# Performance work log

Hardware: AMD Instinct MI355X
Metric: run time of the kernel (lower is better)

## Reference

```python
import jax, jax.numpy as jnp
import numpy as np

H, W, WS, HEADS = 112, 112, 7, 8
DIM, HID = 512, 2048


def _layernorm(x, g, b, eps=1e-5):
    mu = jnp.mean(x, axis=-1, keepdims=True)
    var = jnp.var(x, axis=-1, keepdims=True)
    return (x - mu) * jax.lax.rsqrt(var + eps) * g + b


def _cpe(x, w, b):
    # depthwise 3x3 conv positional encoding with residual; x: [B, L, C]
    B, L, C = x.shape
    img = x.reshape(B, H, W, C)
    feat = jax.lax.conv_general_dilated(
        img, w, window_strides=(1, 1), padding='SAME',
        dimension_numbers=('NHWC', 'HWIO', 'NHWC'), feature_group_count=C) + b
    return x + feat.reshape(B, L, C)


def _window_partition(x):
    # [B, H, W, C] -> [B*nW, ws*ws, C]
    B, _, _, C = x.shape
    x = x.reshape(B, H // WS, WS, W // WS, WS, C)
    x = jnp.transpose(x, (0, 1, 3, 2, 4, 5))
    return x.reshape(-1, WS * WS, C)


def _window_reverse(xw, B):
    # [B*nW, ws*ws, C] -> [B, H*W, C]
    C = xw.shape[-1]
    x = xw.reshape(B, H // WS, W // WS, WS, WS, C)
    x = jnp.transpose(x, (0, 1, 3, 2, 4, 5))
    return x.reshape(B, H * W, C)


def _attention(x, qkv_w, qkv_b, proj_w, proj_b):
    # x: [nW, N, C]; standard MHA within each window
    nW, N, C = x.shape
    d = C // HEADS
    qkv = x @ qkv_w + qkv_b                      # [nW, N, 3C]
    qkv = qkv.reshape(nW, N, 3, HEADS, d)
    q, k, v = qkv[:, :, 0], qkv[:, :, 1], qkv[:, :, 2]  # [nW, N, h, d]
    scale = d ** -0.5
    attn = jnp.einsum('wqhd,wkhd->whqk', q * scale, k)
    attn = jax.nn.softmax(attn, axis=-1)
    out = jnp.einsum('whqk,wkhd->wqhd', attn, v).reshape(nW, N, C)
    return out @ proj_w + proj_b


def setup_inputs() -> dict:
    key = jax.random.key(0)
    ks = jax.random.split(key, 16)
    s = 0.02
    return {
        'x': jax.random.normal(ks[0], (4, H * W, DIM), jnp.float32),
        'cpe0_w': jax.random.normal(ks[1], (3, 3, 1, DIM), jnp.float32) * s,
        'cpe0_b': jnp.zeros((DIM,), jnp.float32),
        'cpe1_w': jax.random.normal(ks[2], (3, 3, 1, DIM), jnp.float32) * s,
        'cpe1_b': jnp.zeros((DIM,), jnp.float32),
        'ln1_g': jnp.ones((DIM,), jnp.float32),
        'ln1_b': jnp.zeros((DIM,), jnp.float32),
        'ln2_g': jnp.ones((DIM,), jnp.float32),
        'ln2_b': jnp.zeros((DIM,), jnp.float32),
        'qkv_w': jax.random.normal(ks[3], (DIM, 3 * DIM), jnp.float32) * s,
        'qkv_b': jnp.zeros((3 * DIM,), jnp.float32),
        'attn_proj_w': jax.random.normal(ks[4], (DIM, DIM), jnp.float32) * s,
        'attn_proj_b': jnp.zeros((DIM,), jnp.float32),
        'fc1_w': jax.random.normal(ks[5], (DIM, HID), jnp.float32) * s,
        'fc1_b': jnp.zeros((HID,), jnp.float32),
        'fc2_w': jax.random.normal(ks[6], (HID, DIM), jnp.float32) * s,
        'fc2_b': jnp.zeros((DIM,), jnp.float32),
    }


def reference(x, cpe0_w, cpe0_b, cpe1_w, cpe1_b, ln1_g, ln1_b, ln2_g, ln2_b,
              qkv_w, qkv_b, attn_proj_w, attn_proj_b, fc1_w, fc1_b, fc2_w, fc2_b):
    B, L, C = x.shape
    shortcut = _cpe(x, cpe0_w, cpe0_b)                 # CPE #1 (with residual)
    h = _layernorm(shortcut, ln1_g, ln1_b)
    h = _window_partition(h.reshape(B, H, W, C))       # [B*nW, 49, C]
    h = _attention(h, qkv_w, qkv_b, attn_proj_w, attn_proj_b)
    h = _window_reverse(h, B)                          # [B, L, C]
    h = shortcut + h
    h = _cpe(h, cpe1_w, cpe1_b)                        # CPE #2 (with residual)
    m = _layernorm(h, ln2_g, ln2_b)
    m = jax.nn.gelu(m @ fc1_w + fc1_b) @ fc2_w + fc2_b
    return h + m
```

## Files before the change

### kernel.cpp

```cpp
#include <hip/hip_runtime.h>
#include <stdint.h>

#define HH 112
#define WW 112
#define CC 512
#define BB 4
#define LLEN (HH*WW)
#define NTOK (BB*LLEN)
#define NHEADS 8
#define HD 64
#define HIDDEN 2048

typedef __bf16 bf16x8 __attribute__((ext_vector_type(8)));
typedef float f32x4 __attribute__((ext_vector_type(4)));
typedef int i32x8 __attribute__((ext_vector_type(8)));
typedef long i64;

__device__ __forceinline__ unsigned short f2bf(float x) {
  uint32_t u = __float_as_uint(x);
  u += 0x7fffu + ((u >> 16) & 1u);
  return (unsigned short)(u >> 16);
}
__device__ __forceinline__ float bf2f(unsigned short h) {
  return __uint_as_float((uint32_t)h << 16);
}
__device__ __forceinline__ int cvt4_fp8(float a, float b, float c, float d) {
  int r = 0;
  r = __builtin_amdgcn_cvt_pk_fp8_f32(a, b, r, false);
  r = __builtin_amdgcn_cvt_pk_fp8_f32(c, d, r, true);
  return r;
}

__device__ __forceinline__ void gload16(const void* gptr, void* lptr) {
  __builtin_amdgcn_global_load_lds(
      (const __attribute__((address_space(1))) void*)gptr,
      (__attribute__((address_space(3))) void*)lptr,
      16, 0, 0);
}

#define WAITV3() asm volatile("s_waitcnt vmcnt(3)" ::: "memory")
#define WAITV4() asm volatile("s_waitcnt vmcnt(4)" ::: "memory")
#define WAITV0() asm volatile("s_waitcnt vmcnt(0)" ::: "memory")
#define BAR() __builtin_amdgcn_s_barrier()
#define WAITL() do { asm volatile("s_waitcnt lgkmcnt(0)" ::: "memory"); \
                     __builtin_amdgcn_sched_barrier(0); } while (0)

__global__ __launch_bounds__(256) void wtall_kernel(
    const float* __restrict__ qkv_w, const float* __restrict__ proj_w,
    const float* __restrict__ fc1_w, const float* __restrict__ fc2_w,
    unsigned char* __restrict__ o0, unsigned char* __restrict__ o1,
    unsigned char* __restrict__ o2, unsigned char* __restrict__ o3) {
  int idx = blockIdx.x * 256 + threadIdx.x;
  const float* w; unsigned char* o; int K, N;
  if (idx < 786432)        { w = qkv_w;  o = o0; K = 512;  N = 1536; }
  else if (idx < 1048576)  { w = proj_w; o = o1; K = 512;  N = 512;  idx -= 786432; }
  else if (idx < 2097152)  { w = fc1_w;  o = o2; K = 512;  N = 2048; idx -= 1048576; }
  else                     { w = fc2_w;  o = o3; K = 2048; N = 512;  idx -= 2097152; }
  int n = idx / K, k = idx - n * K;
  float v = w[(size_t)k * N + n] * 32.f;
  int r = __builtin_amdgcn_cvt_pk_fp8_f32(v, v, 0, false);
  o[idx] = (unsigned char)r;
}

template <int INBF>
__global__ __launch_bounds__(256) void cpe_ln_kernel(
    const void* __restrict__ xin, const float* __restrict__ w,
    const float* __restrict__ bias, const float* __restrict__ lng,
    const float* __restrict__ lnb, unsigned short* __restrict__ outB,
    unsigned char* __restrict__ ln8) {
  const int wid = threadIdx.x >> 6;
  const int lane = threadIdx.x & 63;
  const int xx = blockIdx.x * 4 + wid;
  const int yy = blockIdx.y;
  const int bb = blockIdx.z;
  const int c = lane * 8;

  float acc[8];
  {
    float4 b0 = *(const float4*)(&bias[c]);
    float4 b1 = *(const float4*)(&bias[c + 4]);
    acc[0] = b0.x; acc[1] = b0.y; acc[2] = b0.z; acc[3] = b0.w;
    acc[4] = b1.x; acc[5] = b1.y; acc[6] = b1.z; acc[7] = b1.w;
  }
  float xv[8];

  #pragma unroll
  for (int ky = 0; ky < 3; ky++) {
    int y = yy + ky - 1;
    bool yok = (unsigned)y < (unsigned)HH;
    #pragma unroll
    for (int kx = 0; kx < 3; kx++) {
      int x2 = xx + kx - 1;
      bool ok = yok && ((unsigned)x2 < (unsigned)WW);
      float v[8];
      if (ok) {
        size_t eo = (((size_t)bb * HH + y) * WW + x2) * CC + c;
        if (INBF) {
          uint4 u = *(const uint4*)(&((const unsigned short*)xin)[eo]);
          v[0] = bf2f((unsigned short)(u.x & 0xffff)); v[1] = bf2f((unsigned short)(u.x >> 16));
          v[2] = bf2f((unsigned short)(u.y & 0xffff)); v[3] = bf2f((unsigned short)(u.y >> 16));
          v[4] = bf2f((unsigned short)(u.z & 0xffff)); v[5] = bf2f((unsigned short)(u.z >> 16));
          v[6] = bf2f((unsigned short)(u.w & 0xffff)); v[7] = bf2f((unsigned short)(u.w >> 16));
        } else {
          float4 a = *(const float4*)(&((const float*)xin)[eo]);
          float4 b = *(const float4*)(&((const float*)xin)[eo + 4]);
          v[0] = a.x; v[1] = a.y; v[2] = a.z; v[3] = a.w;
          v[4] = b.x; v[5] = b.y; v[6] = b.z; v[7] = b.w;
        }
      } else {
        #pragma unroll
        for (int e = 0; e < 8; e++) v[e] = 0.f;
      }
      if (ky == 1 && kx == 1) {
        #pragma unroll
        for (int e = 0; e < 8; e++) xv[e] = v[e];
      }
      float4 w0 = *(const float4*)(&w[(ky * 3 + kx) * CC + c]);
      float4 w1 = *(const float4*)(&w[(ky * 3 + kx) * CC + c + 4]);
      acc[0] = fmaf(v[0], w0.x, acc[0]); acc[1] = fmaf(v[1], w0.y, acc[1]);
      acc[2] = fmaf(v[2], w0.z, acc[2]); acc[3] = fmaf(v[3], w0.w, acc[3]);
      acc[4] = fmaf(v[4], w1.x, acc[4]); acc[5] = fmaf(v[5], w1.y, acc[5]);
      acc[6] = fmaf(v[6], w1.z, acc[6]); acc[7] = fmaf(v[7], w1.w, acc[7]);
    }
  }

  float r[8];
  #pragma unroll
  for (int e = 0; e < 8; e++) r[e] = xv[e] + acc[e];

  const size_t o = (((size_t)bb * HH + yy) * WW + xx) * CC + c;
  {
    uint4 pk;
    pk.x = (uint32_t)f2bf(r[0]) | ((uint32_t)f2bf(r[1]) << 16);
    pk.y = (uint32_t)f2bf(r[2]) | ((uint32_t)f2bf(r[3]) << 16);
    pk.z = (uint32_t)f2bf(r[4]) | ((uint32_t)f2bf(r[5]) << 16);
    pk.w = (uint32_t)f2bf(r[6]) | ((uint32_t)f2bf(r[7]) << 16);
    *(uint4*)(&outB[o]) = pk;
  }

  float s = 0.f, ss = 0.f;
  #pragma unroll
  for (int e = 0; e < 8; e++) { s += r[e]; ss += r[e] * r[e]; }
  #pragma unroll
  for (int of = 32; of; of >>= 1) {
    s += __shfl_xor(s, of, 64);
    ss += __shfl_xor(ss, of, 64);
  }
  float mu = s * (1.f / CC);
  float var = ss * (1.f / CC) - mu * mu;
  float rsd = rsqrtf(var + 1e-5f);
  float4 g0 = *(const float4*)(&lng[c]);
  float4 g1 = *(const float4*)(&lng[c + 4]);
  float4 b0 = *(const float4*)(&lnb[c]);
  float4 b1 = *(const float4*)(&lnb[c + 4]);
  float gv[8] = {g0.x, g0.y, g0.z, g0.w, g1.x, g1.y, g1.z, g1.w};
  float bv[8] = {b0.x, b0.y, b0.z, b0.w, b1.x, b1.y, b1.z, b1.w};
  float ov[8];
  #pragma unroll
  for (int e = 0; e < 8; e++) ov[e] = (r[e] - mu) * rsd * gv[e] + bv[e];
  uint2 pk8;
  pk8.x = (uint32_t)cvt4_fp8(ov[0], ov[1], ov[2], ov[3]);
  pk8.y = (uint32_t)cvt4_fp8(ov[4], ov[5], ov[6], ov[7]);
  *(uint2*)(&ln8[o]) = pk8;
}

#define BM 256
#define BN 128
#define BK8 64

template <int MODE, int K>
__global__ __launch_bounds__(512) void gemm8_kernel(
    const unsigned char* __restrict__ A, const unsigned char* __restrict__ BT,
    const float* __restrict__ bias, const unsigned short* __restrict__ resB,
    unsigned short* __restrict__ outB16, int M, int N) {
  __shared__ unsigned char ldsb[49152];
  int nwg = gridDim.x * gridDim.y;
  int flat = blockIdx.y * gridDim.x + blockIdx.x;
  int swz = (flat & 7) * (nwg >> 3) + (flat >> 3);
  int bx = swz % gridDim.x, by = swz / gridDim.x;
  const int bm = by * BM, bn = bx * BN;
  const int t = threadIdx.x;
  const int wid = t >> 6, lane = t & 63;
  const int wr = wid >> 1, wc = wid & 1;
  const int lr = lane & 15, g = lane >> 4;
  const int swr = (lr >> 1) & 3;
  const int rb0 = (((g >> 1)      ) ^ swr) * 16 + (g & 1) * 8;
  const int rb1 = (((g >> 1) + 2) ^ swr) * 16 + (g & 1) * 8;
  const int srow = t >> 2;
  const int scol = (((t & 3) ^ ((t >> 3) & 3)) & 3) * 16;
  const size_t arow0 = (size_t)(bm + srow) * K + scol;
  const size_t arow1 = (size_t)(bm + 128 + srow) * K + scol;
  const size_t brow  = (size_t)(bn + srow) * K + scol;
  const int ldso = wid * 1024;

#define STG8(b, kt) do { \
    gload16(&A[arow0 + (kt)], ldsb + (b) * 16384 + ldso); \
    gload16(&A[arow1 + (kt)], ldsb + (b) * 16384 + 8192 + ldso); \
    gload16(&BT[brow + (kt)], ldsb + 32768 + (b) * 8192 + ldso); } while (0)

  f32x4 acc[4][4] = {};
  constexpr int nt = K / BK8;

  STG8(0, 0);
  STG8(1, BK8);

  #pragma unroll
  for (int tile = 0; tile < nt - 1; ++tile) {
    WAITV3(); BAR();
    const unsigned char* as = ldsb + (tile & 1) * 16384;
    const unsigned char* bs = ldsb + 32768 + (tile & 1) * 8192;
    i64 af0[4], af1[4], bf0[4], bf1[4];
    #pragma unroll
    for (int i = 0; i < 4; i++) {
      const unsigned char* p = &as[(wr * 64 + i * 16 + lr) * BK8];
      af0[i] = *(const i64*)(p + rb0);
      af1[i] = *(const i64*)(p + rb1);
    }
    #pragma unroll
    for (int j = 0; j < 4; j++) {
      const unsigned char* p = &bs[(wc * 64 + j * 16 + lr) * BK8];
      bf0[j] = *(const i64*)(p + rb0);
      bf1[j] = *(const i64*)(p + rb1);
    }
    WAITL();
    BAR();
    if (tile + 2 < nt) STG8(tile & 1, (tile + 2) * BK8);
    __builtin_amdgcn_s_setprio(1);
    #pragma unroll
    for (int i = 0; i < 4; i++)
      #pragma unroll
      for (int j = 0; j < 4; j++) {
        acc[i][j] = __builtin_amdgcn_mfma_f32_16x16x32_fp8_fp8(af0[i], bf0[j], acc[i][j], 0, 0, 0);
        acc[i][j] = __builtin_amdgcn_mfma_f32_16x16x32_fp8_fp8(af1[i], bf1[j], acc[i][j], 0, 0, 0);
      }
    __builtin_amdgcn_s_setprio(0);
  }
  {
    WAITV0(); BAR();
    const unsigned char* as = ldsb + ((nt - 1) & 1) * 16384;
    const unsigned char* bs = ldsb + 32768 + ((nt - 1) & 1) * 8192;
    i64 af0[4], af1[4], bf0[4], bf1[4];
    #pragma unroll
    for (int i = 0; i < 4; i++) {
      const unsigned char* p = &as[(wr * 64 + i * 16 + lr) * BK8];
      af0[i] = *(const i64*)(p + rb0);
      af1[i] = *(const i64*)(p + rb1);
    }
    #pragma unroll
    for (int j = 0; j < 4; j++) {
      const unsigned char* p = &bs[(wc * 64 + j * 16 + lr) * BK8];
      bf0[j] = *(const i64*)(p + rb0);
      bf1[j] = *(const i64*)(p + rb1);
    }
    WAITL();
    #pragma unroll
    for (int i = 0; i < 4; i++)
      #pragma unroll
      for (int j = 0; j < 4; j++) {
        acc[i][j] = __builtin_amdgcn_mfma_f32_16x16x32_fp8_fp8(af0[i], bf0[j], acc[i][j], 0, 0, 0);
        acc[i][j] = __builtin_amdgcn_mfma_f32_16x16x32_fp8_fp8(af1[i], bf1[j], acc[i][j], 0, 0, 0);
      }
  }
#undef STG8

  {
    const float SC = 0.03125f;
    float* eps = (float*)ldsb;
    const int erow = t >> 3;
    const int ecol0 = (t & 7) * 16;
    const int wrow = wr * 16 + (lane >> 4) * 4;
    const int wcol = wc * 64 + lr;
    const int gr_base = bm + (erow >> 4) * 64 + (erow & 15);
    const int gc0 = bn + ecol0;
    float bv[16];
    #pragma unroll
    for (int c4 = 0; c4 < 4; c4++)
      *(float4*)&bv[c4 * 4] = *(const float4*)&bias[gc0 + c4 * 4];
    #pragma unroll
    for (int i = 0; i < 4; i++) {
      __syncthreads();
      #pragma unroll
      for (int j = 0; j < 4; j++)
        #pragma unroll
        for (int r = 0; r < 4; r++)
          eps[(wrow + r) * 132 + wcol + j * 16] = acc[i][j][r];
      __syncthreads();
      float vv[16];
      #pragma unroll
      for (int c4 = 0; c4 < 4; c4++)
        *(float4*)&vv[c4 * 4] = *(const float4*)&eps[erow * 132 + ecol0 + c4 * 4];
      const size_t off = (size_t)(gr_base + i * 16) * N + gc0;
      uint4 r0 = *(const uint4*)&resB[off];
      uint4 r1 = *(const uint4*)&resB[off + 8];
      unsigned short ob[16];
      const uint32_t* rp = (const uint32_t*)&r0;
      #pragma unroll
      for (int c = 0; c < 8; c++) {
        uint32_t u = rp[c >> 1];
        float rv = bf2f((unsigned short)((c & 1) ? (u >> 16) : (u & 0xffff)));
        ob[c] = f2bf(vv[c] * SC + bv[c] + rv);
      }
      const uint32_t* rp1 = (const uint32_t*)&r1;
      #pragma unroll
      for (int c = 0; c < 8; c++) {
        uint32_t u = rp1[c >> 1];
        float rv = bf2f((unsigned short)((c & 1) ? (u >> 16) : (u & 0xffff)));
        ob[8 + c] = f2bf(vv[8 + c] * SC + bv[8 + c] + rv);
      }
      *(uint4*)&outB16[off]     = *(uint4*)&ob[0];
      *(uint4*)&outB16[off + 8] = *(uint4*)&ob[8];
    }
  }
}

__device__ __forceinline__ i32x8 ld_frag128(const unsigned char* base, int row, int g, int lrm7) {
  const uint4 lo = *(const uint4*)(base + row * 128 + (((2 * g)     ^ lrm7) * 16));
  const uint4 hi = *(const uint4*)(base + row * 128 + (((2 * g + 1) ^ lrm7) * 16));
  i32x8 r;
  r[0] = lo.x; r[1] = lo.y; r[2] = lo.z; r[3] = lo.w;
  r[4] = hi.x; r[5] = hi.y; r[6] = hi.z; r[7] = hi.w;
  return r;
}

template <int MODE, int K>
__global__ __launch_bounds__(512) void gemm8mx_kernel(
    const unsigned char* __restrict__ A, const unsigned char* __restrict__ BT,
    const float* __restrict__ bias, const unsigned short* __restrict__ resB,
    float* __restrict__ outF, unsigned char* __restrict__ outB8,
    int M, int N) {
  __shared__ unsigned char ldsb[65536];
  const int SCALE1 = 0x7F7F7F7F;
  int nwg = gridDim.x * gridDim.y;
  int flat = blockIdx.y * gridDim.x + blockIdx.x;
  int swz = (flat & 7) * (nwg >> 3) + (flat >> 3);
  int bx = swz % gridDim.x, by = swz / gridDim.x;
  const int bm = by * 128, bn = bx * 128;
  const int t = threadIdx.x;
  const int wid = t >> 6, lane = t & 63;
  const int wr = wid >> 2, wc = wid & 3;
  const int lr = lane & 15, g = lane >> 4, lrm7 = lane & 7;
  const int srow8 = lane >> 3;
  const int schunk = ((lane & 7) ^ srow8) * 16;
  const size_t aBase = (size_t)(bm + wid * 16 + srow8) * K + schunk;
  const size_t bBase = (size_t)(bn + wid * 16 + srow8) * K + schunk;
  const size_t row8K = (size_t)8 * K;
  const int ldsl = wid * 2048;

#define STGMX(p, kt) do { \
    gload16(&A[aBase + (kt)],          ldsb + (p) * 16384 + ldsl); \
    gload16(&A[aBase + row8K + (kt)],  ldsb + (p) * 16384 + ldsl + 1024); \
    gload16(&BT[bBase + (kt)],         ldsb + 32768 + (p) * 16384 + ldsl); \
    gload16(&BT[bBase + row8K + (kt)], ldsb + 32768 + (p) * 16384 + ldsl + 1024); } while (0)

  f32x4 acc[4][2] = {};
  constexpr int npt = K / 128;

  STGMX(0, 0);
  STGMX(1, 128);

  #pragma unroll
  for (int pt = 0; pt < npt - 1; ++pt) {
    WAITV4(); BAR();
    const unsigned char* as = ldsb + (pt & 1) * 16384;
    const unsigned char* bs = ldsb + 32768 + (pt & 1) * 16384;
    i32x8 af[4], bf[2];
    #pragma unroll
    for (int i = 0; i < 4; i++)
      af[i] = ld_frag128(as, wr * 64 + i * 16 + lr, g, lrm7);
    #pragma unroll
    for (int j = 0; j < 2; j++)
      bf[j] = ld_frag128(bs, wc * 32 + j * 16 + lr, g, lrm7);
    WAITL();
    BAR();
    if (pt + 2 < npt) STGMX(pt & 1, (pt + 2) * 128);
    __builtin_amdgcn_s_setprio(1);
    #pragma unroll
    for (int i = 0; i < 4; i++)
      #pragma unroll
      for (int j = 0; j < 2; j++)
        acc[i][j] = __builtin_amdgcn_mfma_scale_f32_16x16x128_f8f6f4(
            af[i], bf[j], acc[i][j], 0, 0, 0, SCALE1, 0, SCALE1);
    __builtin_amdgcn_s_setprio(0);
  }
  {
    WAITV0(); BAR();
    const unsigned char* as = ldsb + ((npt - 1) & 1) * 16384;
    const unsigned char* bs = ldsb + 32768 + ((npt - 1) & 1) * 16384;
    i32x8 af[4], bf[2];
    #pragma unroll
    for (int i = 0; i < 4; i++)
      af[i] = ld_frag128(as, wr * 64 + i * 16 + lr, g, lrm7);
    #pragma unroll
    for (int j = 0; j < 2; j++)
      bf[j] = ld_frag128(bs, wc * 32 + j * 16 + lr, g, lrm7);
    WAITL();
    #pragma unroll
    for (int i = 0; i < 4; i++)
      #pragma unroll
      for (int j = 0; j < 2; j++)
        acc[i][j] = __builtin_amdgcn_mfma_scale_f32_16x16x128_f8f6f4(
            af[i], bf[j], acc[i][j], 0, 0, 0, SCALE1, 0, SCALE1);
  }
#undef STGMX

  {
    const float SC = 0.03125f;
    float* eps = (float*)ldsb;
    const int erow = t >> 3;
    const int cb = (t & 7) * 16;
    float4 bv4[4];
    #pragma unroll
    for (int c4 = 0; c4 < 4; c4++)
      bv4[c4] = *(const float4*)&bias[bn + cb + c4 * 4];
    #pragma unroll
    for (int p = 0; p < 2; p++) {
      __syncthreads();
      if (wr == p) {
        #pragma unroll
        for (int i = 0; i < 4; i++)
          #pragma unroll
          for (int j = 0; j < 2; j++)
            #pragma unroll
            for (int r = 0; r < 4; r++)
              eps[(i * 16 + g * 4 + r) * 132 + wc * 32 + j * 16 + lr] = acc[i][j][r];
      }
      __syncthreads();
      const size_t rowoff = (size_t)(bm + p * 64 + erow) * N + bn + cb;
      if (MODE == 4) {
        uint4 r0 = *(const uint4*)&resB[rowoff];
        uint4 r1 = *(const uint4*)&resB[rowoff + 8];
        float rvv[16];
        const uint32_t* rp0 = (const uint32_t*)&r0;
        const uint32_t* rp1 = (const uint32_t*)&r1;
        #pragma unroll
        for (int c = 0; c < 8; c++) {
          uint32_t u = rp0[c >> 1];
          rvv[c] = bf2f((unsigned short)((c & 1) ? (u >> 16) : (u & 0xffff)));
        }
        #pragma unroll
        for (int c = 0; c < 8; c++) {
          uint32_t u = rp1[c >> 1];
          rvv[8 + c] = bf2f((unsigned short)((c & 1) ? (u >> 16) : (u & 0xffff)));
        }
        #pragma unroll
        for (int c4 = 0; c4 < 4; c4++) {
          float4 vv = *(const float4*)&eps[erow * 132 + cb + c4 * 4];
          float4 ov;
          ov.x = vv.x * SC + bv4[c4].x + rvv[c4 * 4 + 0];
          ov.y = vv.y * SC + bv4[c4].y + rvv[c4 * 4 + 1];
          ov.z = vv.z * SC + bv4[c4].z + rvv[c4 * 4 + 2];
          ov.w = vv.w * SC + bv4[c4].w + rvv[c4 * 4 + 3];
          *(float4*)&outF[rowoff + c4 * 4] = ov;
        }
      } else {
        uint32_t ob32[4];
        #pragma unroll
        for (int c4 = 0; c4 < 4; c4++) {
          float4 vv = *(const float4*)&eps[erow * 132 + cb + c4 * 4];
          float v0 = vv.x * SC + bv4[c4].x;
          float v1 = vv.y * SC + bv4[c4].y;
          float v2 = vv.z * SC + bv4[c4].z;
          float v3 = vv.w * SC + bv4[c4].w;
          if (MODE == 2) {
            float vin[4] = {v0, v1, v2, v3};
            float gvv[4];
            #pragma unroll
            for (int e = 0; e < 4; e++) {
              float v = vin[e];
              float a2 = v * v;
              float w = v * fmaf(a2, -0.1029436f, -2.3024849f);
              float sg = __builtin_amdgcn_rcpf(1.f + __builtin_amdgcn_exp2f(w));
              gvv[e] = v * sg;
            }
            ob32[c4] = (uint32_t)cvt4_fp8(gvv[0], gvv[1], gvv[2], gvv[3]);
          } else {
            ob32[c4] = (uint32_t)cvt4_fp8(v0, v1, v2, v3);
          }
        }
        *(uint4*)&outB8[rowoff] = *(uint4*)&ob32[0];
      }
    }
  }
}

#define WNS8 72

__global__ __launch_bounds__(64) void attn_mfma8_kernel(
    const unsigned char* __restrict__ qkv, unsigned char* __restrict__ out) {
  __shared__ unsigned char VT[64 * WNS8];
  __shared__ unsigned char Ps[64 * WNS8];
  const int task = blockIdx.x;
  const int win = task >> 3, h = task & 7;
  const int b = win >> 8, wy = (win >> 4) & 15, wx = win & 15;
  const int lane = threadIdx.x;
  const int lr = lane & 15, g = lane >> 4;

  auto tokof = [&](int r) {
    int rr = r > 48 ? 48 : r;
    int y = rr / 7, x2 = rr - y * 7;
    return (size_t)(b * LLEN + (wy * 7 + y) * WW + wx * 7 + x2);
  };

  {
    size_t vbase = tokof(lane) * 1536 + 1024 + h * 64;
    bool valid = lane <= 48;
    #pragma unroll
    for (int c = 0; c < 4; c++) {
      uint4 v = *(const uint4*)(&qkv[vbase + c * 16]);
      const unsigned char* pv = (const unsigned char*)&v;
      #pragma unroll
      for (int e = 0; e < 16; e++)
        VT[(c * 16 + e) * WNS8 + lane] = valid ? pv[e] : (unsigned char)0;
    }
  }

  size_t tok[4];
  #pragma unroll
  for (int i2 = 0; i2 < 4; i2++) tok[i2] = tokof(i2 * 16 + lr);
  i64 Qf[4][2], Kf[4][2];
  #pragma unroll
  for (int i2 = 0; i2 < 4; i2++) {
    size_t base = tok[i2] * 1536 + h * 64 + g * 8;
    #pragma unroll
    for (int ks = 0; ks < 2; ks++) {
      Qf[i2][ks] = *(const i64*)(&qkv[base + ks * 32]);
      Kf[i2][ks] = *(const i64*)(&qkv[base + 512 + ks * 32]);
    }
  }

  f32x4 acc[4][4] = {};
  #pragma unroll
  for (int ks = 0; ks < 2; ks++)
    #pragma unroll
    for (int i2 = 0; i2 < 4; i2++)
      #pragma unroll
      for (int j = 0; j < 4; j++)
        acc[i2][j] = __builtin_amdgcn_mfma_f32_16x16x32_fp8_fp8(Kf[i2][ks], Qf[j][ks], acc[i2][j], 0, 0, 0);

  #pragma unroll
  for (int j = 0; j < 4; j++) {
    float mx = -1e30f;
    #pragma unroll
    for (int i2 = 0; i2 < 4; i2++)
      #pragma unroll
      for (int r = 0; r < 4; r++) {
        int k = 16 * i2 + 4 * g + r;
        mx = fmaxf(mx, (k <= 48) ? acc[i2][j][r] : -1e30f);
      }
    mx = fmaxf(mx, __shfl_xor(mx, 16, 64));
    mx = fmaxf(mx, __shfl_xor(mx, 32, 64));
    float p[4][4];
    float sum = 0.f;
    #pragma unroll
    for (int i2 = 0; i2 < 4; i2++)
      #pragma unroll
      for (int r = 0; r < 4; r++) {
        int k = 16 * i2 + 4 * g + r;
        float e = (k <= 48) ? __expf(0.125f * (acc[i2][j][r] - mx)) : 0.f;
        p[i2][r] = e; sum += e;
      }
    sum += __shfl_xor(sum, 16, 64);
    sum += __shfl_xor(sum, 32, 64);
    float inv = 1.f / sum;
    int q = 16 * j + lr;
    #pragma unroll
    for (int i2 = 0; i2 < 4; i2++) {
      uint32_t w = (uint32_t)cvt4_fp8(p[i2][0] * inv, p[i2][1] * inv,
                                      p[i2][2] * inv, p[i2][3] * inv);
      *(uint32_t*)(&Ps[q * WNS8 + 16 * i2 + 4 * g]) = w;
    }
  }

  __syncthreads();

  f32x4 o[4][4] = {};
  #pragma unroll
  for (int ks = 0; ks < 2; ks++) {
    i64 Pf[4], Vf[4];
    #pragma unroll
    for (int i2 = 0; i2 < 4; i2++)
      Pf[i2] = *(const i64*)(&Ps[(16 * i2 + lr) * WNS8 + ks * 32 + g * 8]);
    #pragma unroll
    for (int j = 0; j < 4; j++)
      Vf[j] = *(const i64*)(&VT[(16 * j + lr) * WNS8 + ks * 32 + g * 8]);
    #pragma unroll
    for (int i2 = 0; i2 < 4; i2++)
      #pragma unroll
      for (int j = 0; j < 4; j++)
        o[i2][j] = __builtin_amdgcn_mfma_f32_16x16x32_fp8_fp8(Pf[i2], Vf[j], o[i2][j], 0, 0, 0);
  }

  #pragma unroll
  for (int i2 = 0; i2 < 4; i2++)
    #pragma unroll
    for (int r = 0; r < 4; r++) {
      int q = 16 * i2 + 4 * g + r;
      if (q <= 48) {
        size_t obase = tokof(q) * 512 + h * 64 + lr;
        #pragma unroll
        for (int j = 0; j < 4; j++) {
          float v = o[i2][j][r];
          int rr = __builtin_amdgcn_cvt_pk_fp8_f32(v, v, 0, false);
          out[obase + 16 * j] = (unsigned char)rr;
        }
      }
    }
}

extern "C" void kernel_launch(void* const* d_in, const int* in_sizes, int n_in,
                              void* d_out, int out_size, void* d_ws, size_t ws_size,
                              hipStream_t stream) {
  const float* x      = (const float*)d_in[0];
  const float* cpe0_w = (const float*)d_in[1];
  const float* cpe0_b = (const float*)d_in[2];
  const float* cpe1_w = (const float*)d_in[3];
  const float* cpe1_b = (const float*)d_in[4];
  const float* ln1_g  = (const float*)d_in[5];
  const float* ln1_b  = (const float*)d_in[6];
  const float* ln2_g  = (const float*)d_in[7];
  const float* ln2_b  = (const float*)d_in[8];
  const float* qkv_w  = (const float*)d_in[9];
  const float* qkv_b  = (const float*)d_in[10];
  const float* proj_w = (const float*)d_in[11];
  const float* proj_b = (const float*)d_in[12];
  const float* fc1_w  = (const float*)d_in[13];
  const float* fc1_b  = (const float*)d_in[14];
  const float* fc2_w  = (const float*)d_in[15];
  const float* fc2_b  = (const float*)d_in[16];
  float* out = (float*)d_out;
  char* ws = (char*)d_ws;

  unsigned char*  qkvwT8  = (unsigned char*)(ws + 0);
  unsigned char*  projwT8 = (unsigned char*)(ws + 1048576);
  unsigned char*  fc1wT8  = (unsigned char*)(ws + 2097152);
  unsigned char*  fc2wT8  = (unsigned char*)(ws + 4194304);
  unsigned short* shortcB = (unsigned short*)(ws + 6291456);
  unsigned char*  lnb8    = (unsigned char*)(ws + 109051904);
  unsigned char*  qkvb8   = (unsigned char*)(ws + 160432128);
  unsigned char*  attnb8  = (unsigned char*)(ws + 314572800);
  unsigned char*  gelub8  = (unsigned char*)(ws + 160432128);
  unsigned short* h2B     = (unsigned short*)(ws + 314572800);

  wtall_kernel<<<12288, 256, 0, stream>>>(qkv_w, proj_w, fc1_w, fc2_w,
                                          qkvwT8, projwT8, fc1wT8, fc2wT8);

  cpe_ln_kernel<0><<<dim3(28, 112, BB), 256, 0, stream>>>(x, cpe0_w, cpe0_b,
      ln1_g, ln1_b, shortcB, lnb8);
  gemm8mx_kernel<0, 512><<<dim3(12, 392), 512, 0, stream>>>(lnb8, qkvwT8, qkv_b,
      nullptr, nullptr, qkvb8, NTOK, 1536);
  attn_mfma8_kernel<<<8192, 64, 0, stream>>>(qkvb8, attnb8);
  gemm8_kernel<3, 512><<<dim3(4, 196), 512, 0, stream>>>(attnb8, projwT8, proj_b,
      shortcB, shortcB, NTOK, 512);
  cpe_ln_kernel<1><<<dim3(28, 112, BB), 256, 0, stream>>>(shortcB, cpe1_w, cpe1_b,
      ln2_g, ln2_b, h2B, lnb8);
  gemm8mx_kernel<2, 512><<<dim3(16, 392), 512, 0, stream>>>(lnb8, fc1wT8, fc1_b,
      nullptr, nullptr, gelub8, NTOK, 2048);
  gemm8mx_kernel<4, 2048><<<dim3(4, 392), 512, 0, stream>>>(gelub8, fc2wT8, fc2_b,
      h2B, out, nullptr, NTOK, 512);
}
```

Baseline: 517.1 us.

## Load GEMM B fragments directly from global memory, stage only A in LDS

The FP8 MFMA GEMM no longer stages the weight (B) tile through shared memory. Each wave now reads its B fragments straight from global memory into registers every k-step, and only A is double-buffered via global_load_lds. This cuts LDS use from 64KB to about 33KB, halves the staging loads per iteration and folds the tail iteration into the main loop. The trade-off is that B loads are no longer prefetched ahead of time, so their global or L2 latency may be exposed right before the MFMAs. Each wave also re-reads B rows that other waves share, adding redundant cache traffic.

```diff
diff --git a/kernel.cpp b/kernel.cpp
--- a/kernel.cpp
+++ b/kernel.cpp
@@ -39,7 +39,7 @@
 }
 
 #define WAITV3() asm volatile("s_waitcnt vmcnt(3)" ::: "memory")
-#define WAITV4() asm volatile("s_waitcnt vmcnt(4)" ::: "memory")
+#define WAITV2() asm volatile("s_waitcnt vmcnt(2)" ::: "memory")
 #define WAITV0() asm volatile("s_waitcnt vmcnt(0)" ::: "memory")
 #define BAR() __builtin_amdgcn_s_barrier()
 #define WAITL() do { asm volatile("s_waitcnt lgkmcnt(0)" ::: "memory"); \
@@ -328,7 +328,7 @@
     const float* __restrict__ bias, const unsigned short* __restrict__ resB,
     float* __restrict__ outF, unsigned char* __restrict__ outB8,
     int M, int N) {
-  __shared__ unsigned char ldsb[65536];
+  __shared__ unsigned char ldsb[33792];
   const int SCALE1 = 0x7F7F7F7F;
   int nwg = gridDim.x * gridDim.y;
   int flat = blockIdx.y * gridDim.x + blockIdx.x;
@@ -342,15 +342,14 @@
   const int srow8 = lane >> 3;
   const int schunk = ((lane & 7) ^ srow8) * 16;
   const size_t aBase = (size_t)(bm + wid * 16 + srow8) * K + schunk;
-  const size_t bBase = (size_t)(bn + wid * 16 + srow8) * K + schunk;
   const size_t row8K = (size_t)8 * K;
   const int ldsl = wid * 2048;
+  const unsigned char* bPtr = BT + (size_t)(bn + wc * 32 + lr) * K + g * 32;
+  const size_t bRow16 = (size_t)16 * K;
 
 #define STGMX(p, kt) do { \
     gload16(&A[aBase + (kt)],          ldsb + (p) * 16384 + ldsl); \
-    gload16(&A[aBase + row8K + (kt)],  ldsb + (p) * 16384 + ldsl + 1024); \
-    gload16(&BT[bBase + (kt)],         ldsb + 32768 + (p) * 16384 + ldsl); \
-    gload16(&BT[bBase + row8K + (kt)], ldsb + 32768 + (p) * 16384 + ldsl + 1024); } while (0)
+    gload16(&A[aBase + row8K + (kt)],  ldsb + (p) * 16384 + ldsl + 1024); } while (0)
 
   f32x4 acc[4][2] = {};
   constexpr int npt = K / 128;
@@ -359,17 +358,23 @@
   STGMX(1, 128);
 
   #pragma unroll
-  for (int pt = 0; pt < npt - 1; ++pt) {
-    WAITV4(); BAR();
+  for (int pt = 0; pt < npt; ++pt) {
+    if (pt < npt - 1) { WAITV2(); } else { WAITV0(); }
+    BAR();
     const unsigned char* as = ldsb + (pt & 1) * 16384;
-    const unsigned char* bs = ldsb + 32768 + (pt & 1) * 16384;
-    i32x8 af[4], bf[2];
+    i32x8 bf[2];
+    #pragma unroll
+    for (int j = 0; j < 2; j++) {
+      const unsigned char* p = bPtr + (size_t)j * bRow16 + pt * 128;
+      uint4 lo = *(const uint4*)(p);
+      uint4 hi = *(const uint4*)(p + 16);
+      bf[j][0] = lo.x; bf[j][1] = lo.y; bf[j][2] = lo.z; bf[j][3] = lo.w;
+      bf[j][4] = hi.x; bf[j][5] = hi.y; bf[j][6] = hi.z; bf[j][7] = hi.w;
+    }
+    i32x8 af[4];
     #pragma unroll
     for (int i = 0; i < 4; i++)
       af[i] = ld_frag128(as, wr * 64 + i * 16 + lr, g, lrm7);
-    #pragma unroll
-    for (int j = 0; j < 2; j++)
-      bf[j] = ld_frag128(bs, wc * 32 + j * 16 + lr, g, lrm7);
     WAITL();
     BAR();
     if (pt + 2 < npt) STGMX(pt & 1, (pt + 2) * 128);
@@ -381,25 +386,6 @@
         acc[i][j] = __builtin_amdgcn_mfma_scale_f32_16x16x128_f8f6f4(
             af[i], bf[j], acc[i][j], 0, 0, 0, SCALE1, 0, SCALE1);
     __builtin_amdgcn_s_setprio(0);
-  }
-  {
-    WAITV0(); BAR();
-    const unsigned char* as = ldsb + ((npt - 1) & 1) * 16384;
-    const unsigned char* bs = ldsb + 32768 + ((npt - 1) & 1) * 16384;
-    i32x8 af[4], bf[2];
-    #pragma unroll
-    for (int i = 0; i < 4; i++)
-      af[i] = ld_frag128(as, wr * 64 + i * 16 + lr, g, lrm7);
-    #pragma unroll
-    for (int j = 0; j < 2; j++)
-      bf[j] = ld_frag128(bs, wc * 32 + j * 16 + lr, g, lrm7);
-    WAITL();
-    #pragma unroll
-    for (int i = 0; i < 4; i++)
-      #pragma unroll
-      for (int j = 0; j < 2; j++)
-        acc[i][j] = __builtin_amdgcn_mfma_scale_f32_16x16x128_f8f6f4(
-            af[i], bf[j], acc[i][j], 0, 0, 0, SCALE1, 0, SCALE1);
   }
 #undef STGMX
 
```

New measurement: 665.2 us. 1.29x slower.
